# Kernel tuning notes

Measured on AMD Instinct MI355X. Metric: run time of the kernel, lower is better.

The kernel has to match this reference:

```python
import jax, jax.numpy as jnp
import numpy as np

DIM = 2
N_SIGMA = 2
THRESHOLD = 0.5
MIN_PIXEL = 160
MIN_INST_PIXEL = 160
MIN_SEED_THRESH = 0.5
INST_RATIO = 0.5
DIST_THRESH = 0.5
MAX_COUNT = 200


def setup_inputs() -> dict:
    key = jax.random.key(0)
    # scale 0.1 keeps sigma near 0 so exp(10*sigma)~O(1) and proposals are
    # realistically sized (same regime as a trained network's outputs).
    prediction = 0.1 * jax.random.normal(key, (1, 7, 1024, 2048), dtype=jnp.float32)
    return {"prediction": prediction}


def _forward(prediction):
    pred = prediction[0]                       # [C, H, W]
    H, W = pred.shape[1], pred.shape[2]
    # coordinate grid (larger=False: x in [0,2] over 2048, y in [0,1] over 1024)
    xm = jnp.linspace(0.0, 2.0, 2048)[:W]
    ym = jnp.linspace(0.0, 1.0, 1024)[:H]
    xym = jnp.stack([jnp.broadcast_to(xm[None, :], (H, W)),
                     jnp.broadcast_to(ym[:, None], (H, W))], axis=0)  # [2,H,W]

    spatial_emb = jnp.tanh(pred[0:DIM]) + xym               # [2,H,W]
    sigma = pred[DIM:DIM + N_SIGMA]                         # [2,H,W]
    seed = jax.nn.softmax(pred[DIM + 1 + N_SIGMA:DIM + N_SIGMA + 3], axis=0)[1]  # [H,W]

    N = H * W
    se = spatial_emb.reshape(DIM, N)
    sg = sigma.reshape(N_SIGMA, N)
    sm = seed.reshape(N)
    m = sm > MIN_SEED_THRESH                                # candidate-pixel mask

    unclustered0 = m.astype(jnp.float32)
    inst0 = jnp.zeros((N,), jnp.int32)
    prev0 = jnp.zeros((MAX_COUNT,), jnp.int32)              # proposal size at assignment time

    def cond(state):
        unclustered, inst, count, prev, stopped = state
        return (~stopped) & (jnp.sum(unclustered) > MIN_PIXEL) & (count < MAX_COUNT)

    def body(state):
        unclustered, inst, count, prev, stopped = state
        scores = sm * unclustered
        seed_idx = jnp.argmax(scores)
        seed_score = scores[seed_idx]
        stop_now = seed_score < THRESHOLD                   # == break in torch loop

        center = se[:, seed_idx]                            # [2]
        s = jnp.exp(sg[:, seed_idx] * 10.0)                 # [2]
        # exp(-sum((emb - center)^2 * s)) over all pixels; AND with mask m to
        # match torch (which only computes over masked pixels)
        dist = jnp.exp(-jnp.sum((se - center[:, None]) ** 2 * s[:, None], axis=0))
        proposal = (dist > DIST_THRESH) & m                 # [N] bool

        uncl = unclustered.at[seed_idx].set(0.0)            # unclustered[seed]=0
        prop_sum = jnp.sum(proposal)
        uncl_in_prop = jnp.sum(uncl * proposal)
        accept = (prop_sum > MIN_INST_PIXEL) & (
            uncl_in_prop / jnp.maximum(prop_sum.astype(jnp.float32), 1.0) > INST_RATIO)

        inst_new = jnp.where(accept & proposal, count, inst)
        prev_new = jnp.where(accept, prev.at[count].set(prop_sum), prev)
        count_new = jnp.where(accept, count + 1, count)
        uncl_new = jnp.where(proposal, 0.0, uncl)           # always consume proposal

        # if the seed score fell below threshold, revert and stop (break)
        return (jnp.where(stop_now, unclustered, uncl_new),
                jnp.where(stop_now, inst, inst_new),
                jnp.where(stop_now, count, count_new),
                jnp.where(stop_now, prev, prev_new),
                stop_now)

    state = (unclustered0, inst0, jnp.int32(1), prev0, jnp.array(False))
    unclustered, inst, count, prev, _ = jax.lax.while_loop(cond, body, state)

    # dropped if too small or too eroded
    now = jnp.bincount(inst, length=MAX_COUNT).astype(jnp.int32)
    ratio = now.astype(jnp.float32) / jnp.maximum(prev, 1).astype(jnp.float32)
    bad = (now != prev) & (now > 0) & ((now < MIN_INST_PIXEL * 3) | (ratio < INST_RATIO))
    bad = bad.at[0].set(False)                              # background never removed
    inst = jnp.where(bad[inst], 0, inst)
    return inst.reshape(H, W).astype(jnp.uint8)[None]       # [1,H,W]


def reference(prediction):
    return _forward(prediction)
```

## Files before the change

kernel.cpp:

```cpp
#include <hip/hip_runtime.h>
#include <cstddef>

typedef unsigned long long ull;

#define NPIX (1024 * 2048)
#define WW 2048
#define MAXC 200
#define GRIDB 256
#define BLKT 1024
#define PXT 8
#define TAGSH 52
#define DMASK ((1ull << TAGSH) - 1)
#define TCAP 2000

union F8 { float4 v[2]; float f[8]; };
union I8 { int4 v[2]; int f[8]; };

__device__ inline ull AL(ull* p) { return __hip_atomic_load(p, __ATOMIC_RELAXED, __HIP_MEMORY_SCOPE_AGENT); }
__device__ inline void AS(ull* p, ull v) { __hip_atomic_store(p, v, __ATOMIC_RELAXED, __HIP_MEMORY_SCOPE_AGENT); }
__device__ inline void ASI(int* p, int v) { __hip_atomic_store(p, v, __ATOMIC_RELAXED, __HIP_MEMORY_SCOPE_AGENT); }
__device__ inline int ALI(int* p) { return __hip_atomic_load(p, __ATOMIC_RELAXED, __HIP_MEMORY_SCOPE_AGENT); }

__device__ inline ull shfl_down_u64(ull v, int o) {
  unsigned lo = (unsigned)v, hi = (unsigned)(v >> 32);
  lo = __shfl_down(lo, o, 64);
  hi = __shfl_down(hi, o, 64);
  return ((ull)hi << 32) | lo;
}

__device__ inline void tup_wred(ull& k, ull& x, ull& y, ull& w, ull& z) {
  #pragma unroll
  for (int o = 32; o > 0; o >>= 1) {
    ull k2 = shfl_down_u64(k, o), x2 = shfl_down_u64(x, o), y2 = shfl_down_u64(y, o),
        w2 = shfl_down_u64(w, o), z2 = shfl_down_u64(z, o);
    if (k2 > k) { k = k2; x = x2; y = y2; w = w2; }
    z += z2;
  }
}

__device__ inline void pack3(float c0, float c1, float e0, float e1, ull& X, ull& Y, ull& W) {
  ull b0 = __float_as_uint(c0), b1 = __float_as_uint(c1),
      b2 = __float_as_uint(e0), b3 = __float_as_uint(e1);
  X = (b0 << 20) | (b1 >> 12);
  Y = ((b1 & 0xFFFull) << 40) | (b2 << 8) | (b3 >> 24);
  W = (b3 & 0xFFFFFFull) << 28;
}

__device__ inline ull pk_arg(float sc, int idx) {
  return ((ull)__float_as_uint(sc) << 21) | (ull)(0x1FFFFFu - (unsigned)idx);
}

__global__ __launch_bounds__(BLKT) void k_all(
    const float* __restrict__ pred,
    ull* __restrict__ slots,
    int* __restrict__ prevp, int* __restrict__ nowp,
    int* __restrict__ out)
{
  __shared__ ull lsa[4][5];
  __shared__ ull lsb[16][5];
  __shared__ int lbad[MAXC];

  const int b = blockIdx.x;
  const int tid = threadIdx.x;
  const int wid = tid >> 6, lane = tid & 63;
  const int base = (b * BLKT + tid) * PXT;

  F8 Av, Bv, Sv, E0, E1;
  ull iv = 0;
  ull pp = 0;
  {
    F8 P0, P1, P2, P3, P5, P6;
    P0.v[0] = *(const float4*)(pred + base);            P0.v[1] = *(const float4*)(pred + base + 4);
    P1.v[0] = *(const float4*)(pred + NPIX + base);     P1.v[1] = *(const float4*)(pred + NPIX + base + 4);
    P2.v[0] = *(const float4*)(pred + 2 * NPIX + base); P2.v[1] = *(const float4*)(pred + 2 * NPIX + base + 4);
    P3.v[0] = *(const float4*)(pred + 3 * NPIX + base); P3.v[1] = *(const float4*)(pred + 3 * NPIX + base + 4);
    P5.v[0] = *(const float4*)(pred + 5 * NPIX + base); P5.v[1] = *(const float4*)(pred + 5 * NPIX + base + 4);
    P6.v[0] = *(const float4*)(pred + 6 * NPIX + base); P6.v[1] = *(const float4*)(pred + 6 * NPIX + base + 4);
    const int h = base >> 11;
    const int wb = base & (WW - 1);
    const float yv = __fmul_rn((float)h, 1.0f / 1023.0f);
    int cnt = 0;
    ull best = 0; float bc0 = 0, bc1 = 0, be0 = 0, be1 = 0;
    #pragma unroll
    for (int j = 0; j < PXT; j++) {
      Av.f[j] = __fadd_rn(tanhf(P0.f[j]), __fmul_rn((float)(wb + j), 2.0f / 2047.0f));
      Bv.f[j] = __fadd_rn(tanhf(P1.f[j]), yv);
      E0.f[j] = expf(__fmul_rn(P2.f[j], 10.0f));
      E1.f[j] = expf(__fmul_rn(P3.f[j], 10.0f));
      float a = P5.f[j], bb = P6.f[j];
      float mx = fmaxf(a, bb);
      float ea = expf(__fsub_rn(a, mx));
      float eb = expf(__fsub_rn(bb, mx));
      float s = __fdiv_rn(eb, __fadd_rn(ea, eb));
      Sv.f[j] = s;
      cnt += (s > 0.5f) ? 1 : 0;
      float sc = (s > 0.5f) ? s : 0.0f;
      ull pk = pk_arg(sc, base + j);
      if (pk > best) { best = pk; bc0 = Av.f[j]; bc1 = Bv.f[j]; be0 = E0.f[j]; be1 = E1.f[j]; }
    }
    ull px, py, pw;
    pack3(bc0, bc1, be0, be1, px, py, pw);
    ull pz = ((ull)(unsigned)cnt << 26);
    ull pk_ = best;
    tup_wred(pk_, px, py, pw, pz);
    if (lane == 0) { lsb[wid][0] = pk_; lsb[wid][1] = px; lsb[wid][2] = py; lsb[wid][3] = pw; lsb[wid][4] = pz; }
    if (b == 0) {
      for (int c = tid; c < MAXC; c += BLKT) { ASI(&nowp[c], 0); ASI(&prevp[c], 0); }
    }
    __syncthreads();
    if (tid == 0) {
      ull K2 = lsb[0][0], X2 = lsb[0][1], Y2 = lsb[0][2], W2 = lsb[0][3], Z2 = lsb[0][4];
      for (int i = 1; i < 16; i++) {
        ull kk = lsb[i][0];
        if (kk > K2) { K2 = kk; X2 = lsb[i][1]; Y2 = lsb[i][2]; W2 = lsb[i][3]; }
        Z2 += lsb[i][4];
      }
      ull* sl = slots + b * 8;
      AS(sl + 4, Z2); AS(sl + 3, W2); AS(sl + 2, Y2); AS(sl + 1, X2); AS(sl + 0, K2);
    }
  }

  int count = 1, rem = 0, tstop = 0;
  for (int t = 0; t < TCAP; ++t) {
    const unsigned tg = (unsigned)t;
    if (tid < GRIDB) {
      ull* sl = slots + tid * 8;
      ull k, x, y, w, z;
      for (;;) {
        k = AL(sl + 0); x = AL(sl + 1); y = AL(sl + 2); w = AL(sl + 3); z = AL(sl + 4);
        if (((unsigned)(k >> TAGSH) == tg) & ((unsigned)(x >> TAGSH) == tg) &
            ((unsigned)(y >> TAGSH) == tg) & ((unsigned)(w >> TAGSH) == tg) &
            ((unsigned)(z >> TAGSH) == tg)) break;
      }
      k &= DMASK; x &= DMASK; y &= DMASK; w &= DMASK; z &= DMASK;
      tup_wred(k, x, y, w, z);
      if (lane == 0) { lsa[wid][0] = k; lsa[wid][1] = x; lsa[wid][2] = y; lsa[wid][3] = w; lsa[wid][4] = z; }
    }
    __syncthreads();
    ull K = lsa[0][0], X = lsa[0][1], Y = lsa[0][2], W = lsa[0][3], Z = lsa[0][4];
    #pragma unroll
    for (int i = 1; i < 4; i++) {
      ull kk = lsa[i][0], xx = lsa[i][1], yy = lsa[i][2], ww = lsa[i][3], zz = lsa[i][4];
      if (kk > K) { K = kk; X = xx; Y = yy; W = ww; }
      Z += zz;
    }
    const int psS = (int)((Z >> 26) & 0x3FFFFFF), uipS = (int)(Z & 0x3FFFFFF);
    bool accP = false; int labP = 0;
    if (t == 0) {
      rem = psS;
    } else {
      accP = (psS > 160) &&
             (__fdiv_rn((float)uipS, fmaxf((float)psS, 1.0f)) > 0.5f);
      labP = count;
      if (accP) {
        if (b == 0 && tid == 0) ASI(&prevp[count], psS);
        count++;
      }
      rem -= (1 + uipS);
    }
    if (accP && pp)
      iv = (iv & ~(pp * 0xFFull)) | (pp * (ull)(unsigned)labP);
    const float score = __uint_as_float((unsigned)((K >> 21) & 0x7FFFFFFF));
    const int sidx = 0x1FFFFF - (int)(K & 0x1FFFFF);
    if (!((rem > 160) && (count < MAXC)) || (score < 0.5f)) { tstop = t; break; }

    const float c0 = __uint_as_float((unsigned)((X >> 20) & 0xFFFFFFFFull));
    const float c1 = __uint_as_float((unsigned)(((X & 0xFFFFFull) << 12) | ((Y >> 40) & 0xFFFull)));
    const float s0 = __uint_as_float((unsigned)((Y >> 8) & 0xFFFFFFFFull));
    const float s1 = __uint_as_float((unsigned)(((Y & 0xFFull) << 24) | ((W >> 28) & 0xFFFFFFull)));

    ull best = 0, npp = 0;
    int psl = 0, uipl = 0;
    float bc0 = 0, bc1 = 0, be0 = 0, be1 = 0;
    #pragma unroll
    for (int j = 0; j < PXT; j++) {
      float d0 = __fsub_rn(Av.f[j], c0);
      float d1 = __fsub_rn(Bv.f[j], c1);
      float tt = __fadd_rn(__fmul_rn(__fmul_rn(d0, d0), s0),
                           __fmul_rn(__fmul_rn(d1, d1), s1));
      float dist = expf(-tt);
      float s = Sv.f[j];
      bool pr = (dist > 0.5f) && (fabsf(s) > 0.5f);
      if (pr) {
        npp |= (0x01ull << (8 * j));
        psl++;
        if (s > 0.5f) {
          if ((base + j) != sidx) uipl++;
          s = -s; Sv.f[j] = s;
        }
      }
      float sc = (s > 0.5f) ? s : 0.0f;
      ull pk = pk_arg(sc, base + j);
      if (pk > best) { best = pk; bc0 = Av.f[j]; bc1 = Bv.f[j]; be0 = E0.f[j]; be1 = E1.f[j]; }
    }
    pp = npp;

    ull px, py, pw;
    pack3(bc0, bc1, be0, be1, px, py, pw);
    ull pz = ((ull)(unsigned)psl << 26) | (ull)(unsigned)uipl;
    ull pk_ = best;
    tup_wred(pk_, px, py, pw, pz);
    if (lane == 0) { lsb[wid][0] = pk_; lsb[wid][1] = px; lsb[wid][2] = py; lsb[wid][3] = pw; lsb[wid][4] = pz; }
    __syncthreads();
    if (tid == 0) {
      ull K2 = lsb[0][0], X2 = lsb[0][1], Y2 = lsb[0][2], W2 = lsb[0][3], Z2 = lsb[0][4];
      for (int i = 1; i < 16; i++) {
        ull kk = lsb[i][0];
        if (kk > K2) { K2 = kk; X2 = lsb[i][1]; Y2 = lsb[i][2]; W2 = lsb[i][3]; }
        Z2 += lsb[i][4];
      }
      const ull tagw = ((ull)(unsigned)(t + 1)) << TAGSH;
      ull* sl = slots + b * 8;
      AS(sl + 4, tagw | Z2); AS(sl + 3, tagw | W2); AS(sl + 2, tagw | Y2);
      AS(sl + 1, tagw | X2); AS(sl + 0, tagw | K2);
    }
  }

  for (int c = tid; c < MAXC; c += BLKT) lbad[c] = 0;
  __syncthreads();
  {
    int cur = -1, acc = 0;
    #pragma unroll
    for (int j = 0; j < PXT; j++) {
      int lb = (int)((iv >> (8 * j)) & 0xFFull);
      if (lb == cur) { acc++; }
      else { if (cur > 0) atomicAdd(&lbad[cur], acc); cur = lb; acc = 1; }
    }
    if (cur > 0) atomicAdd(&lbad[cur], acc);
  }
  __syncthreads();
  for (int c = tid + 1; c < MAXC; c += BLKT)
    if (lbad[c]) atomicAdd(&nowp[c], lbad[c]);
  __syncthreads();
  {
    const unsigned etg = (unsigned)(tstop + 1);
    if (tid == 0) AS(slots + b * 8, ((ull)etg) << TAGSH);
    if (tid < GRIDB) {
      ull* sl = slots + tid * 8;
      while ((unsigned)(AL(sl) >> TAGSH) != etg) {}
    }
  }
  __syncthreads();
  if (tid < MAXC) {
    int c = tid;
    int nw = (c == 0) ? 0 : ALI(&nowp[c]);
    int pv = ALI(&prevp[c]);
    float ratio = __fdiv_rn((float)nw, (float)(pv > 1 ? pv : 1));
    int bd = (nw != pv) && (nw > 0) && ((nw < 3 * 160) || (ratio < 0.5f));
    if (c == 0) bd = 0;
    lbad[c] = bd;
  }
  __syncthreads();
  {
    I8 O;
    #pragma unroll
    for (int j = 0; j < PXT; j++) {
      int v = (int)((iv >> (8 * j)) & 0xFFull);
      O.f[j] = lbad[v] ? 0 : v;
    }
    *(int4*)(out + base) = O.v[0];
    *(int4*)(out + base + 4) = O.v[1];
  }
}

extern "C" void kernel_launch(void* const* d_in, const int* in_sizes, int n_in,
                              void* d_out, int out_size, void* d_ws, size_t ws_size,
                              hipStream_t stream) {
  const float* pred = (const float*)d_in[0];
  char* ws = (char*)d_ws;
  size_t off = 0;
  ull* slots = (ull*)(ws + off); off += (size_t)GRIDB * 8 * sizeof(ull);
  int* prevp = (int*)(ws + off); off += MAXC * sizeof(int);
  int* nowp  = (int*)(ws + off); off += MAXC * sizeof(int);
  int* out = (int*)d_out;

  hipLaunchKernelGGL(k_all, dim3(GRIDB), dim3(BLKT), 0, stream,
                     pred, slots, prevp, nowp, out);
}
```

Baseline: 52.05 us.

## Shrink cross-block exchange to argmax key and counts, recompute seed params

Each block now publishes only two 64-bit words per iteration, the argmax key and the packed counts, instead of five. Seed center and sigma are recomputed from the prediction tensor at the winning index rather than carried through the reductions. Blocks become 512 threads with 16 pixels each, and E0/E1 registers are dropped. This targets the per-iteration cost of the grid-wide handshake and the shuffle reductions, at the price of four dependent global loads plus tanh and exp on the serial path each iteration, and fewer warps per block.

```diff
diff --git a/kernel.cpp b/kernel.cpp
--- a/kernel.cpp
+++ b/kernel.cpp
@@ -7,14 +7,15 @@
 #define WW 2048
 #define MAXC 200
 #define GRIDB 256
-#define BLKT 1024
-#define PXT 8
-#define TAGSH 52
+#define BLKT 512
+#define PXT 16
+#define NW (BLKT / 64)
+#define TAGSH 56
 #define DMASK ((1ull << TAGSH) - 1)
-#define TCAP 2000
-
-union F8 { float4 v[2]; float f[8]; };
-union I8 { int4 v[2]; int f[8]; };
+#define TCAP 250
+
+union F16x { float4 v[4]; float f[16]; };
+union I16x { int4 v[4]; int f[16]; };
 
 __device__ inline ull AL(ull* p) { return __hip_atomic_load(p, __ATOMIC_RELAXED, __HIP_MEMORY_SCOPE_AGENT); }
 __device__ inline void AS(ull* p, ull v) { __hip_atomic_store(p, v, __ATOMIC_RELAXED, __HIP_MEMORY_SCOPE_AGENT); }
@@ -27,151 +28,141 @@
   hi = __shfl_down(hi, o, 64);
   return ((ull)hi << 32) | lo;
 }
-
-__device__ inline void tup_wred(ull& k, ull& x, ull& y, ull& w, ull& z) {
+__device__ inline void wred_kz(ull& k, ull& z) {
   #pragma unroll
   for (int o = 32; o > 0; o >>= 1) {
-    ull k2 = shfl_down_u64(k, o), x2 = shfl_down_u64(x, o), y2 = shfl_down_u64(y, o),
-        w2 = shfl_down_u64(w, o), z2 = shfl_down_u64(z, o);
-    if (k2 > k) { k = k2; x = x2; y = y2; w = w2; }
+    ull k2 = shfl_down_u64(k, o), z2 = shfl_down_u64(z, o);
+    if (k2 > k) k = k2;
     z += z2;
   }
 }
 
-__device__ inline void pack3(float c0, float c1, float e0, float e1, ull& X, ull& Y, ull& W) {
-  ull b0 = __float_as_uint(c0), b1 = __float_as_uint(c1),
-      b2 = __float_as_uint(e0), b3 = __float_as_uint(e1);
-  X = (b0 << 20) | (b1 >> 12);
-  Y = ((b1 & 0xFFFull) << 40) | (b2 << 8) | (b3 >> 24);
-  W = (b3 & 0xFFFFFFull) << 28;
-}
-
-__device__ inline ull pk_arg(float sc, int idx) {
-  return ((ull)__float_as_uint(sc) << 21) | (ull)(0x1FFFFFu - (unsigned)idx);
-}
-
-__global__ __launch_bounds__(BLKT) void k_all(
+__global__ __launch_bounds__(BLKT, 1) void k_all(
     const float* __restrict__ pred,
     ull* __restrict__ slots,
     int* __restrict__ prevp, int* __restrict__ nowp,
     int* __restrict__ out)
 {
-  __shared__ ull lsa[4][5];
-  __shared__ ull lsb[16][5];
+  __shared__ ull lsaK[4], lsaZ[4];
+  __shared__ ull lsbK[NW], lsbZ[NW];
   __shared__ int lbad[MAXC];
 
-  const int b = blockIdx.x;
-  const int tid = threadIdx.x;
+  const int b = blockIdx.x, tid = threadIdx.x;
   const int wid = tid >> 6, lane = tid & 63;
   const int base = (b * BLKT + tid) * PXT;
-
-  F8 Av, Bv, Sv, E0, E1;
-  ull iv = 0;
-  ull pp = 0;
-  {
-    F8 P0, P1, P2, P3, P5, P6;
-    P0.v[0] = *(const float4*)(pred + base);            P0.v[1] = *(const float4*)(pred + base + 4);
-    P1.v[0] = *(const float4*)(pred + NPIX + base);     P1.v[1] = *(const float4*)(pred + NPIX + base + 4);
-    P2.v[0] = *(const float4*)(pred + 2 * NPIX + base); P2.v[1] = *(const float4*)(pred + 2 * NPIX + base + 4);
-    P3.v[0] = *(const float4*)(pred + 3 * NPIX + base); P3.v[1] = *(const float4*)(pred + 3 * NPIX + base + 4);
-    P5.v[0] = *(const float4*)(pred + 5 * NPIX + base); P5.v[1] = *(const float4*)(pred + 5 * NPIX + base + 4);
-    P6.v[0] = *(const float4*)(pred + 6 * NPIX + base); P6.v[1] = *(const float4*)(pred + 6 * NPIX + base + 4);
-    const int h = base >> 11;
-    const int wb = base & (WW - 1);
-    const float yv = __fmul_rn((float)h, 1.0f / 1023.0f);
-    int cnt = 0;
-    ull best = 0; float bc0 = 0, bc1 = 0, be0 = 0, be1 = 0;
-    #pragma unroll
-    for (int j = 0; j < PXT; j++) {
-      Av.f[j] = __fadd_rn(tanhf(P0.f[j]), __fmul_rn((float)(wb + j), 2.0f / 2047.0f));
-      Bv.f[j] = __fadd_rn(tanhf(P1.f[j]), yv);
-      E0.f[j] = expf(__fmul_rn(P2.f[j], 10.0f));
-      E1.f[j] = expf(__fmul_rn(P3.f[j], 10.0f));
-      float a = P5.f[j], bb = P6.f[j];
+  const float dxs = 2.0f / 2047.0f;
+  const float dys = 1.0f / 1023.0f;
+
+  F16x Av, Bv, Sv;
+  ull iv0 = 0, iv1 = 0;
+  unsigned pp = 0;
+
+  {
+    F16x P, Q;
+    const int h = base >> 11, wb = base & (WW - 1);
+    const float yv = __fmul_rn((float)h, dys);
+    #pragma unroll
+    for (int q = 0; q < 4; q++) P.v[q] = *(const float4*)(pred + base + 4 * q);
+    #pragma unroll
+    for (int j = 0; j < PXT; j++)
+      Av.f[j] = __fadd_rn(tanhf(P.f[j]), __fmul_rn((float)(wb + j), dxs));
+    #pragma unroll
+    for (int q = 0; q < 4; q++) P.v[q] = *(const float4*)(pred + NPIX + base + 4 * q);
+    #pragma unroll
+    for (int j = 0; j < PXT; j++)
+      Bv.f[j] = __fadd_rn(tanhf(P.f[j]), yv);
+    #pragma unroll
+    for (int q = 0; q < 4; q++) P.v[q] = *(const float4*)(pred + 5 * NPIX + base + 4 * q);
+    #pragma unroll
+    for (int q = 0; q < 4; q++) Q.v[q] = *(const float4*)(pred + 6 * NPIX + base + 4 * q);
+    #pragma unroll
+    for (int j = 0; j < PXT; j++) {
+      float a = P.f[j], bb = Q.f[j];
       float mx = fmaxf(a, bb);
       float ea = expf(__fsub_rn(a, mx));
       float eb = expf(__fsub_rn(bb, mx));
-      float s = __fdiv_rn(eb, __fadd_rn(ea, eb));
-      Sv.f[j] = s;
+      Sv.f[j] = __fdiv_rn(eb, __fadd_rn(ea, eb));
+    }
+    ull bk = 0; int cnt = 0;
+    #pragma unroll
+    for (int j = 0; j < PXT; j++) {
+      float s = Sv.f[j];
       cnt += (s > 0.5f) ? 1 : 0;
       float sc = (s > 0.5f) ? s : 0.0f;
-      ull pk = pk_arg(sc, base + j);
-      if (pk > best) { best = pk; bc0 = Av.f[j]; bc1 = Bv.f[j]; be0 = E0.f[j]; be1 = E1.f[j]; }
-    }
-    ull px, py, pw;
-    pack3(bc0, bc1, be0, be1, px, py, pw);
-    ull pz = ((ull)(unsigned)cnt << 26);
-    ull pk_ = best;
-    tup_wred(pk_, px, py, pw, pz);
-    if (lane == 0) { lsb[wid][0] = pk_; lsb[wid][1] = px; lsb[wid][2] = py; lsb[wid][3] = pw; lsb[wid][4] = pz; }
-    if (b == 0) {
+      ull pk = ((ull)__float_as_uint(sc) << 21) | (ull)(0x1FFFFFu - (unsigned)(base + j));
+      if (pk > bk) bk = pk;
+    }
+    ull bz = ((ull)(unsigned)cnt) << 24;
+    wred_kz(bk, bz);
+    if (lane == 0) { lsbK[wid] = bk; lsbZ[wid] = bz; }
+    if (b == 0)
       for (int c = tid; c < MAXC; c += BLKT) { ASI(&nowp[c], 0); ASI(&prevp[c], 0); }
-    }
     __syncthreads();
     if (tid == 0) {
-      ull K2 = lsb[0][0], X2 = lsb[0][1], Y2 = lsb[0][2], W2 = lsb[0][3], Z2 = lsb[0][4];
-      for (int i = 1; i < 16; i++) {
-        ull kk = lsb[i][0];
-        if (kk > K2) { K2 = kk; X2 = lsb[i][1]; Y2 = lsb[i][2]; W2 = lsb[i][3]; }
-        Z2 += lsb[i][4];
+      ull K = lsbK[0], Z = lsbZ[0];
+      for (int i = 1; i < NW; i++) { if (lsbK[i] > K) K = lsbK[i]; Z += lsbZ[i]; }
+      const ull tw = 1ull << TAGSH;
+      AS(&slots[b * 8 + 1], tw | Z);
+      AS(&slots[b * 8 + 0], tw | K);
+    }
+  }
+
+  int count = 1, rem = 0, tstop = 0;
+  for (int t = 0;; ++t) {
+    const unsigned tg = (unsigned)(t + 1) & 0xFFu;
+    if (tid < GRIDB) {
+      ull* sl = &slots[tid * 8];
+      ull k, z;
+      for (;;) {
+        k = AL(sl); z = AL(sl + 1);
+        if (((unsigned)(k >> TAGSH) == tg) & ((unsigned)(z >> TAGSH) == tg)) break;
       }
-      ull* sl = slots + b * 8;
-      AS(sl + 4, Z2); AS(sl + 3, W2); AS(sl + 2, Y2); AS(sl + 1, X2); AS(sl + 0, K2);
-    }
-  }
-
-  int count = 1, rem = 0, tstop = 0;
-  for (int t = 0; t < TCAP; ++t) {
-    const unsigned tg = (unsigned)t;
-    if (tid < GRIDB) {
-      ull* sl = slots + tid * 8;
-      ull k, x, y, w, z;
-      for (;;) {
-        k = AL(sl + 0); x = AL(sl + 1); y = AL(sl + 2); w = AL(sl + 3); z = AL(sl + 4);
-        if (((unsigned)(k >> TAGSH) == tg) & ((unsigned)(x >> TAGSH) == tg) &
-            ((unsigned)(y >> TAGSH) == tg) & ((unsigned)(w >> TAGSH) == tg) &
-            ((unsigned)(z >> TAGSH) == tg)) break;
-      }
-      k &= DMASK; x &= DMASK; y &= DMASK; w &= DMASK; z &= DMASK;
-      tup_wred(k, x, y, w, z);
-      if (lane == 0) { lsa[wid][0] = k; lsa[wid][1] = x; lsa[wid][2] = y; lsa[wid][3] = w; lsa[wid][4] = z; }
+      k &= DMASK; z &= DMASK;
+      wred_kz(k, z);
+      if (lane == 0) { lsaK[wid] = k; lsaZ[wid] = z; }
     }
     __syncthreads();
-    ull K = lsa[0][0], X = lsa[0][1], Y = lsa[0][2], W = lsa[0][3], Z = lsa[0][4];
-    #pragma unroll
-    for (int i = 1; i < 4; i++) {
-      ull kk = lsa[i][0], xx = lsa[i][1], yy = lsa[i][2], ww = lsa[i][3], zz = lsa[i][4];
-      if (kk > K) { K = kk; X = xx; Y = yy; W = ww; }
-      Z += zz;
-    }
-    const int psS = (int)((Z >> 26) & 0x3FFFFFF), uipS = (int)(Z & 0x3FFFFFF);
+    ull K = lsaK[0], Z = lsaZ[0];
+    #pragma unroll
+    for (int i = 1; i < 4; i++) { ull kk = lsaK[i]; if (kk > K) K = kk; Z += lsaZ[i]; }
+
     bool accP = false; int labP = 0;
     if (t == 0) {
-      rem = psS;
+      rem = (int)(Z >> 24);
     } else {
-      accP = (psS > 160) &&
-             (__fdiv_rn((float)uipS, fmaxf((float)psS, 1.0f)) > 0.5f);
-      labP = count;
+      int ps = (int)((Z >> 24) & 0xFFFFFF), ui = (int)(Z & 0xFFFFFF);
+      accP = (ps > 160) &&
+             (__fdiv_rn((float)(ui - 1), fmaxf((float)ps, 1.0f)) > 0.5f);
       if (accP) {
-        if (b == 0 && tid == 0) ASI(&prevp[count], psS);
+        labP = count;
+        if (b == 0 && tid == 0) ASI(&prevp[count], ps);
         count++;
       }
-      rem -= (1 + uipS);
-    }
-    if (accP && pp)
-      iv = (iv & ~(pp * 0xFFull)) | (pp * (ull)(unsigned)labP);
+      rem -= ui;
+    }
+    if (accP && pp) {
+      #pragma unroll
+      for (int j = 0; j < 8; j++)
+        if ((pp >> j) & 1) iv0 = (iv0 & ~(0xFFull << (8 * j))) | ((ull)(unsigned)labP << (8 * j));
+      #pragma unroll
+      for (int j = 0; j < 8; j++)
+        if ((pp >> (8 + j)) & 1) iv1 = (iv1 & ~(0xFFull << (8 * j))) | ((ull)(unsigned)labP << (8 * j));
+    }
+    if (!((rem > 160) && (count < MAXC))) { tstop = t; break; }
     const float score = __uint_as_float((unsigned)((K >> 21) & 0x7FFFFFFF));
+    if (score < 0.5f) { tstop = t; break; }
     const int sidx = 0x1FFFFF - (int)(K & 0x1FFFFF);
-    if (!((rem > 160) && (count < MAXC)) || (score < 0.5f)) { tstop = t; break; }
-
-    const float c0 = __uint_as_float((unsigned)((X >> 20) & 0xFFFFFFFFull));
-    const float c1 = __uint_as_float((unsigned)(((X & 0xFFFFFull) << 12) | ((Y >> 40) & 0xFFFull)));
-    const float s0 = __uint_as_float((unsigned)((Y >> 8) & 0xFFFFFFFFull));
-    const float s1 = __uint_as_float((unsigned)(((Y & 0xFFull) << 24) | ((W >> 28) & 0xFFFFFFull)));
-
-    ull best = 0, npp = 0;
-    int psl = 0, uipl = 0;
-    float bc0 = 0, bc1 = 0, be0 = 0, be1 = 0;
+
+    const float p0 = pred[sidx];
+    const float p1 = pred[NPIX + sidx];
+    const float p2 = pred[2 * NPIX + sidx];
+    const float p3 = pred[3 * NPIX + sidx];
+    const float c0 = __fadd_rn(tanhf(p0), __fmul_rn((float)(sidx & (WW - 1)), dxs));
+    const float c1 = __fadd_rn(tanhf(p1), __fmul_rn((float)(sidx >> 11), dys));
+    const float s0 = expf(__fmul_rn(p2, 10.0f));
+    const float s1 = expf(__fmul_rn(p3, 10.0f));
+
+    ull bk = 0; int psl = 0, uil = 0; unsigned ppn = 0;
     #pragma unroll
     for (int j = 0; j < PXT; j++) {
       float d0 = __fsub_rn(Av.f[j], c0);
@@ -182,38 +173,27 @@
       float s = Sv.f[j];
       bool pr = (dist > 0.5f) && (fabsf(s) > 0.5f);
       if (pr) {
-        npp |= (0x01ull << (8 * j));
+        ppn |= 1u << j;
         psl++;
-        if (s > 0.5f) {
-          if ((base + j) != sidx) uipl++;
-          s = -s; Sv.f[j] = s;
-        }
+        if (s > 0.5f) { uil++; s = -s; Sv.f[j] = s; }
       }
       float sc = (s > 0.5f) ? s : 0.0f;
-      ull pk = pk_arg(sc, base + j);
-      if (pk > best) { best = pk; bc0 = Av.f[j]; bc1 = Bv.f[j]; be0 = E0.f[j]; be1 = E1.f[j]; }
-    }
-    pp = npp;
-
-    ull px, py, pw;
-    pack3(bc0, bc1, be0, be1, px, py, pw);
-    ull pz = ((ull)(unsigned)psl << 26) | (ull)(unsigned)uipl;
-    ull pk_ = best;
-    tup_wred(pk_, px, py, pw, pz);
-    if (lane == 0) { lsb[wid][0] = pk_; lsb[wid][1] = px; lsb[wid][2] = py; lsb[wid][3] = pw; lsb[wid][4] = pz; }
+      ull pk = ((ull)__float_as_uint(sc) << 21) | (ull)(0x1FFFFFu - (unsigned)(base + j));
+      if (pk > bk) bk = pk;
+    }
+    pp = ppn;
+    ull bz = ((ull)(unsigned)psl << 24) | (unsigned)uil;
+    wred_kz(bk, bz);
+    if (lane == 0) { lsbK[wid] = bk; lsbZ[wid] = bz; }
     __syncthreads();
     if (tid == 0) {
-      ull K2 = lsb[0][0], X2 = lsb[0][1], Y2 = lsb[0][2], W2 = lsb[0][3], Z2 = lsb[0][4];
-      for (int i = 1; i < 16; i++) {
-        ull kk = lsb[i][0];
-        if (kk > K2) { K2 = kk; X2 = lsb[i][1]; Y2 = lsb[i][2]; W2 = lsb[i][3]; }
-        Z2 += lsb[i][4];
-      }
-      const ull tagw = ((ull)(unsigned)(t + 1)) << TAGSH;
-      ull* sl = slots + b * 8;
-      AS(sl + 4, tagw | Z2); AS(sl + 3, tagw | W2); AS(sl + 2, tagw | Y2);
-      AS(sl + 1, tagw | X2); AS(sl + 0, tagw | K2);
-    }
+      ull K2 = lsbK[0], Z2 = lsbZ[0];
+      for (int i = 1; i < NW; i++) { if (lsbK[i] > K2) K2 = lsbK[i]; Z2 += lsbZ[i]; }
+      const ull tw = ((ull)((unsigned)(t + 2) & 0xFFu)) << TAGSH;
+      AS(&slots[b * 8 + 1], tw | Z2);
+      AS(&slots[b * 8 + 0], tw | K2);
+    }
+    if (t + 1 >= TCAP) { tstop = t + 1; break; }
   }
 
   for (int c = tid; c < MAXC; c += BLKT) lbad[c] = 0;
@@ -222,8 +202,8 @@
     int cur = -1, acc = 0;
     #pragma unroll
     for (int j = 0; j < PXT; j++) {
-      int lb = (int)((iv >> (8 * j)) & 0xFFull);
-      if (lb == cur) { acc++; }
+      int lb = (int)(((j < 8) ? (iv0 >> (8 * j)) : (iv1 >> (8 * (j - 8)))) & 0xFF);
+      if (lb == cur) acc++;
       else { if (cur > 0) atomicAdd(&lbad[cur], acc); cur = lb; acc = 1; }
     }
     if (cur > 0) atomicAdd(&lbad[cur], acc);
@@ -233,11 +213,14 @@
     if (lbad[c]) atomicAdd(&nowp[c], lbad[c]);
   __syncthreads();
   {
-    const unsigned etg = (unsigned)(tstop + 1);
-    if (tid == 0) AS(slots + b * 8, ((ull)etg) << TAGSH);
+    const unsigned etg = (unsigned)(tstop + 2) & 0xFFu;
+    if (tid == 0)
+      __hip_atomic_store(&slots[b * 8], ((ull)etg) << TAGSH,
+                         __ATOMIC_RELEASE, __HIP_MEMORY_SCOPE_AGENT);
     if (tid < GRIDB) {
-      ull* sl = slots + tid * 8;
-      while ((unsigned)(AL(sl) >> TAGSH) != etg) {}
+      ull* sl = &slots[tid * 8];
+      while ((unsigned)(__hip_atomic_load(sl, __ATOMIC_ACQUIRE,
+                                          __HIP_MEMORY_SCOPE_AGENT) >> TAGSH) != etg) {}
     }
   }
   __syncthreads();
@@ -252,14 +235,14 @@
   }
   __syncthreads();
   {
-    I8 O;
-    #pragma unroll
-    for (int j = 0; j < PXT; j++) {
-      int v = (int)((iv >> (8 * j)) & 0xFFull);
+    I16x O;
+    #pragma unroll
+    for (int j = 0; j < PXT; j++) {
+      int v = (int)(((j < 8) ? (iv0 >> (8 * j)) : (iv1 >> (8 * (j - 8)))) & 0xFF);
       O.f[j] = lbad[v] ? 0 : v;
     }
-    *(int4*)(out + base) = O.v[0];
-    *(int4*)(out + base + 4) = O.v[1];
+    #pragma unroll
+    for (int q = 0; q < 4; q++) *(int4*)(out + base + 4 * q) = O.v[q];
   }
 }
 
```

Measured after the change: 53.07 us. No clear change (+2.0%).
